# Performance work log

Measured on AMD Instinct MI355X. Metric: run time of the kernel, lower is better.

Reference implementation:

```python
import jax, jax.numpy as jnp
import numpy as np

B, C, H, W = 16, 1536, 32, 32
M = 64      # num_clusters
L = 128     # cluster_dim
G = 256     # token_dim
HID = 512
OT_ITERS = 3
EPS = 1e-6


def setup_inputs() -> dict:
    key = jax.random.key(0)
    ks = jax.random.split(key, 12)
    def w(k, shape, fan_in):
        return jax.random.normal(k, shape, jnp.float32) * (1.0 / np.sqrt(fan_in))
    return {
        'x': jax.random.normal(ks[0], (B, C, H, W), jnp.float32),
        't': jax.random.normal(ks[1], (B, C), jnp.float32),
        # token_features: Linear(C->512), ReLU, Linear(512->G)
        'Wt1': w(ks[2], (HID, C), C), 'bt1': jnp.zeros((HID,), jnp.float32),
        'Wt2': w(ks[3], (G, HID), HID), 'bt2': jnp.zeros((G,), jnp.float32),
        # cluster_features: 1x1 Conv(C->512), ReLU, 1x1 Conv(512->L)
        'Wc1': w(ks[4], (HID, C), C), 'bc1': jnp.zeros((HID,), jnp.float32),
        'Wc2': w(ks[5], (L, HID), HID), 'bc2': jnp.zeros((L,), jnp.float32),
        # score: 1x1 Conv(C->512), ReLU, 1x1 Conv(512->M)
        'Ws1': w(ks[6], (HID, C), C), 'bs1': jnp.zeros((HID,), jnp.float32),
        'Ws2': w(ks[7], (M, HID), HID), 'bs2': jnp.zeros((M,), jnp.float32),
        # temp_predictor: Conv1d(L->1, k=1)
        'Wtp': w(ks[8], (L,), L), 'btp': jnp.zeros((), jnp.float32),
        'dust_bin': jnp.asarray(1.0, jnp.float32),
        'burst_b': jnp.asarray(0.0, jnp.float32),
        'burst_p': jnp.asarray(1.0, jnp.float32),
        'lambda_discount': jnp.asarray(0.5, jnp.float32),
    }


def _log_optimal_transport(scores, alpha, iters):
    # scores: [B, m, n]; alpha: scalar dust-bin logit
    b, m, n = scores.shape
    Z0 = jnp.concatenate([scores, jnp.broadcast_to(alpha, (b, 1, n))], axis=1)  # [B, m+1, n]
    norm = -jnp.log(jnp.asarray(m + n, scores.dtype))
    log_mu = jnp.concatenate([jnp.full((m,), norm, scores.dtype),
                              (jnp.log(jnp.asarray(n, scores.dtype)) + norm)[None]])  # [m+1]
    log_nu = jnp.full((n,), norm, scores.dtype)
    u = jnp.zeros((b, m + 1), scores.dtype)
    v = jnp.zeros((b, n), scores.dtype)
    for _ in range(iters):
        u = log_mu - jax.nn.logsumexp(Z0 + v[:, None, :], axis=2)
        v = log_nu - jax.nn.logsumexp(Z0 + u[:, :, None], axis=1)
    return Z0 + u[:, :, None] + v[:, None, :] - norm


def _l2norm(a, axis):
    return a / jnp.maximum(jnp.linalg.norm(a, axis=axis, keepdims=True), 1e-12)


def _forward(x, t, Wt1, bt1, Wt2, bt2, Wc1, bc1, Wc2, bc2, Ws1, bs1, Ws2, bs2,
             Wtp, btp, dust_bin, burst_b, burst_p, lambda_discount):
    b, c, h, w = x.shape
    n = h * w
    xf = x.reshape(b, c, n)  # [B, C, N] (1x1 convs == per-pixel MLP)
    # cluster features f: [B, L, N]
    h1 = jax.nn.relu(jnp.einsum('bcn,oc->bon', xf, Wc1) + bc1[:, None])
    f = jnp.einsum('bhn,lh->bln', h1, Wc2) + bc2[:, None]
    # assignment scores p: [B, M, N]
    h2 = jax.nn.relu(jnp.einsum('bcn,oc->bon', xf, Ws1) + bs1[:, None])
    p = jnp.einsum('bhn,mh->bmn', h2, Ws2) + bs2[:, None]
    # global token: [B, G]
    tok = jax.nn.relu(t @ Wt1.T + bt1) @ Wt2.T + bt2
    # Sinkhorn OT soft assignment, drop dust bin row
    P = jnp.exp(_log_optimal_transport(p, dust_bin, OT_ITERS))[:, :-1, :]  # [B, M, N]
    # burst-aware weighting
    f_norm = _l2norm(f, axis=1)                                  # [B, L, N]
    T_i = jax.nn.softplus(jnp.einsum('bln,l->bn', f, Wtp) + btp)  # [B, N]
    sim = jnp.einsum('bli,blj->bij', f_norm, f_norm)              # [B, N, N]
    T_avg = (T_i[:, :, None] + T_i[:, None, :]) * 0.5
    burst_w = jax.nn.sigmoid(T_avg * sim + burst_b)
    discount = jnp.clip(jnp.sum(burst_w, axis=-1) ** burst_p, 1e-3, 1e3)  # [B, N]
    lam = jax.nn.sigmoid(lambda_discount)
    P_adj = (1.0 - lam) * P + lam * (P / (discount[:, None, :] + EPS))
    # local aggregation: (f[:, :, None, :] * P[:, None, :, :]).sum(-1) == batched matmul
    agg = jnp.einsum('bln,bmn->blm', f, P_adj)  # [B, L, M]
    agg = _l2norm(agg, axis=1).reshape(b, -1)   # [B, L*M]
    tok_n = _l2norm(tok, axis=-1)
    g = jnp.concatenate([tok_n, agg], axis=-1)  # [B, G + L*M]
    return _l2norm(g, axis=-1)


def reference(x, t, Wt1, bt1, Wt2, bt2, Wc1, bc1, Wc2, bc2, Ws1, bs1, Ws2, bs2,
              Wtp, btp, dust_bin, burst_b, burst_p, lambda_discount):
    return _forward(x, t, Wt1, bt1, Wt2, bt2, Wc1, bc1, Wc2, bc2, Ws1, bs1, Ws2, bs2,
                    Wtp, btp, dust_bin, burst_b, burst_p, lambda_discount)
```

## Files before the change

### kernel.cpp

```cpp
#include <hip/hip_runtime.h>
#include <math.h>

#define B_   16
#define C_   1536
#define N_   1024
#define M_   64
#define L_   128
#define G_   256
#define HID_ 512

typedef __attribute__((ext_vector_type(8))) short short8;
typedef __attribute__((ext_vector_type(4))) float floatx4;

__device__ __forceinline__ unsigned short f2bf_rne(float x) {
    unsigned u = __float_as_uint(x);
    unsigned r = u + 0x7fffu + ((u >> 16) & 1u);
    return (unsigned short)(r >> 16);
}
__device__ __forceinline__ unsigned pack_bf2(float lo, float hi) {
    unsigned a = __float_as_uint(lo) + 0x8000u;
    unsigned b = __float_as_uint(hi) + 0x8000u;
    return (a >> 16) | (b & 0xffff0000u);
}

__device__ __forceinline__ void gl2lds16(const void* g, void* l) {
    __builtin_amdgcn_global_load_lds(
        (const __attribute__((address_space(1))) void*)g,
        (__attribute__((address_space(3))) void*)l, 16, 0, 0);
}

__global__ __launch_bounds__(256) void cast_w_kernel(
    const float* __restrict__ Wc1, const float* __restrict__ Ws1,
    const float* __restrict__ Wc2, const float* __restrict__ Ws2,
    unsigned short* __restrict__ Wbf, unsigned short* __restrict__ W2)
{
    const int T1 = 1024 * 1536;
    int idx = blockIdx.x * 256 + threadIdx.x;
    if (idx < T1) {
        float v = (idx < 512 * 1536) ? Wc1[idx] : Ws1[idx - 512 * 1536];
        Wbf[idx] = f2bf_rne(v);
    } else if (idx < T1 + 192 * 1024) {
        int i2 = idx - T1;
        int row = i2 >> 10, k = i2 & 1023;
        float v = 0.f;
        if (row < 128) { if (k < 512) v = Wc2[row * 512 + k]; }
        else           { if (k >= 512) v = Ws2[(row - 128) * 512 + (k - 512)]; }
        W2[i2] = f2bf_rne(v);
    }
}

__global__ __launch_bounds__(256) void xt_kernel(
    const float* __restrict__ x, unsigned short* __restrict__ xT, int bofs)
{
    __shared__ float Xs[64][65];
    const int t = threadIdx.x;
    const int n0 = blockIdx.x * 64, c0 = blockIdx.y * 64, bl = blockIdx.z;
    const float* xb = x + (long)(bofs + bl) * C_ * N_;
    #pragma unroll
    for (int it = 0; it < 16; ++it) {
        int idx = it * 256 + t, cr = idx >> 6, nc = idx & 63;
        Xs[cr][nc] = xb[(long)(c0 + cr) * N_ + n0 + nc];
    }
    __syncthreads();
    unsigned* xo = (unsigned*)(xT + (long)bl * N_ * C_);
    #pragma unroll
    for (int it = 0; it < 8; ++it) {
        int idx = it * 256 + t, nr = idx >> 5, pc = idx & 31;
        xo[(long)(n0 + nr) * 768 + (c0 >> 1) + pc] =
            pack_bf2(Xs[2 * pc][nr], Xs[2 * pc + 1][nr]);
    }
}

__global__ __launch_bounds__(256, 2) void gemm1_kernel(
    const unsigned short* __restrict__ Wbf, const unsigned short* __restrict__ xT,
    const float* __restrict__ bc1, const float* __restrict__ bs1,
    unsigned short* __restrict__ hT, int bofs)
{
    __shared__ unsigned short As[128 * 32];
    __shared__ unsigned short Bs[128 * 32];
    const int t = threadIdx.x;
    const int lane = t & 63, w = t >> 6;
    const int n0 = blockIdx.x * 128, o0 = blockIdx.y * 128;
    const int bl = blockIdx.z, bg = bofs + bl;
    const unsigned short* xb = xT + (long)bl * N_ * C_;

    const int wo = (w >> 1) * 64, wn = (w & 1) * 64;
    const int lrow = lane & 15, kgrp = lane >> 4;
    const int arow = t >> 2, acol = (t & 3) * 8;

    floatx4 acc[4][4];
    #pragma unroll
    for (int i = 0; i < 4; ++i)
        #pragma unroll
        for (int j = 0; j < 4; ++j) acc[i][j] = (floatx4)0.0f;

    for (int k0 = 0; k0 < C_; k0 += 32) {
        #pragma unroll
        for (int r = 0; r < 2; ++r)
            gl2lds16(Wbf + (long)(o0 + r * 64 + arow) * C_ + k0 + acol,
                     (char*)As + r * 4096 + t * 16);
        #pragma unroll
        for (int r = 0; r < 2; ++r)
            gl2lds16(xb + (long)(n0 + r * 64 + arow) * C_ + k0 + acol,
                     (char*)Bs + r * 4096 + t * 16);
        __syncthreads();
        short8 af[4], bfr[4];
        #pragma unroll
        for (int i = 0; i < 4; ++i)
            af[i] = *(const short8*)((const char*)As +
                        (wo + i * 16 + lrow) * 64 + kgrp * 16);
        #pragma unroll
        for (int j = 0; j < 4; ++j)
            bfr[j] = *(const short8*)((const char*)Bs +
                        (wn + j * 16 + lrow) * 64 + kgrp * 16);
        #pragma unroll
        for (int i = 0; i < 4; ++i)
            #pragma unroll
            for (int j = 0; j < 4; ++j)
                acc[i][j] = __builtin_amdgcn_mfma_f32_16x16x32_bf16(
                    af[i], bfr[j], acc[i][j], 0, 0, 0);
        __syncthreads();
    }

    const float* bias = (o0 < 512) ? bc1 : bs1;
    const int ob = (o0 < 512) ? o0 : o0 - 512;
    #pragma unroll
    for (int i = 0; i < 4; ++i) {
        int orow = wo + i * 16 + kgrp * 4;
        float b0 = bias[ob + orow + 0], b1 = bias[ob + orow + 1];
        float b2 = bias[ob + orow + 2], b3 = bias[ob + orow + 3];
        #pragma unroll
        for (int j = 0; j < 4; ++j) {
            int n = n0 + wn + j * 16 + lrow;
            float v0 = fmaxf(acc[i][j][0] + b0, 0.f);
            float v1 = fmaxf(acc[i][j][1] + b1, 0.f);
            float v2 = fmaxf(acc[i][j][2] + b2, 0.f);
            float v3 = fmaxf(acc[i][j][3] + b3, 0.f);
            uint2 pk;
            pk.x = ((unsigned)f2bf_rne(v0)) | (((unsigned)f2bf_rne(v1)) << 16);
            pk.y = ((unsigned)f2bf_rne(v2)) | (((unsigned)f2bf_rne(v3)) << 16);
            *(uint2*)&hT[((long)bg * N_ + n) * 1024 + o0 + orow] = pk;
        }
    }
}

__global__ __launch_bounds__(256, 2) void gemm23_kernel(
    const unsigned short* __restrict__ W2, const unsigned short* __restrict__ hT,
    const float* __restrict__ bc2, const float* __restrict__ bs2,
    float* __restrict__ f, float* __restrict__ p)
{
    __shared__ unsigned short As[64 * 32];
    __shared__ unsigned short Bs[128 * 32];
    const int t = threadIdx.x;
    const int lane = t & 63, w = t >> 6;
    const int n0 = blockIdx.x * 128, o0 = blockIdx.y * 64, b = blockIdx.z;
    const unsigned short* hTb = hT + (long)b * N_ * 1024;

    const int wo = (w >> 1) * 32, wn = (w & 1) * 64;
    const int lrow = lane & 15, kgrp = lane >> 4;
    const int arow = t >> 2, acol = (t & 3) * 8;

    floatx4 acc[2][4];
    #pragma unroll
    for (int i = 0; i < 2; ++i)
        #pragma unroll
        for (int j = 0; j < 4; ++j) acc[i][j] = (floatx4)0.0f;

    for (int k0 = 0; k0 < 1024; k0 += 32) {
        gl2lds16(W2 + (long)(o0 + arow) * 1024 + k0 + acol, (char*)As + t * 16);
        #pragma unroll
        for (int r = 0; r < 2; ++r)
            gl2lds16(hTb + (long)(n0 + r * 64 + arow) * 1024 + k0 + acol,
                     (char*)Bs + r * 4096 + t * 16);
        __syncthreads();
        short8 af[2], bfr[4];
        #pragma unroll
        for (int i = 0; i < 2; ++i)
            af[i] = *(const short8*)((const char*)As +
                        (wo + i * 16 + lrow) * 64 + kgrp * 16);
        #pragma unroll
        for (int j = 0; j < 4; ++j)
            bfr[j] = *(const short8*)((const char*)Bs +
                        (wn + j * 16 + lrow) * 64 + kgrp * 16);
        #pragma unroll
        for (int i = 0; i < 2; ++i)
            #pragma unroll
            for (int j = 0; j < 4; ++j)
                acc[i][j] = __builtin_amdgcn_mfma_f32_16x16x32_bf16(
                    af[i], bfr[j], acc[i][j], 0, 0, 0);
        __syncthreads();
    }

    #pragma unroll
    for (int i = 0; i < 2; ++i) {
        int o = o0 + wo + i * 16 + kgrp * 4;
        #pragma unroll
        for (int j = 0; j < 4; ++j) {
            int n = n0 + wn + j * 16 + lrow;
            #pragma unroll
            for (int r = 0; r < 4; ++r) {
                int oo = o + r;
                float v = acc[i][j][r];
                if (oo < 128) f[((long)b * L_ + oo) * N_ + n] = v + bc2[oo];
                else p[((long)b * M_ + (oo - 128)) * N_ + n] = v + bs2[oo - 128];
            }
        }
    }
}

__global__ __launch_bounds__(256) void token1_kernel(
    const float* __restrict__ t_in, const float* __restrict__ Wt1,
    const float* __restrict__ bt1, float* __restrict__ hid)
{
    const int lane = threadIdx.x & 63, w = threadIdx.x >> 6;
    const int o = blockIdx.x * 4 + w, b = blockIdx.y;
    const float4* wr = (const float4*)(Wt1 + (long)o * C_);
    const float4* tb = (const float4*)(t_in + (long)b * C_);
    float acc = 0.f;
    #pragma unroll
    for (int i = 0; i < 6; ++i) {
        float4 a = wr[i * 64 + lane], tv = tb[i * 64 + lane];
        acc += a.x * tv.x + a.y * tv.y + a.z * tv.z + a.w * tv.w;
    }
    #pragma unroll
    for (int off = 1; off < 64; off <<= 1) acc += __shfl_xor(acc, off);
    if (lane == 0) hid[b * HID_ + o] = fmaxf(acc + bt1[o], 0.f);
}

__global__ __launch_bounds__(256) void token2_kernel(
    const float* __restrict__ hid, const float* __restrict__ Wt2,
    const float* __restrict__ bt2, float* __restrict__ tok)
{
    const int lane = threadIdx.x & 63, w = threadIdx.x >> 6;
    const int g = blockIdx.x * 4 + w, b = blockIdx.y;
    const float4* wr = (const float4*)(Wt2 + (long)g * HID_);
    const float4* hb = (const float4*)(hid + (long)b * HID_);
    float acc = 0.f;
    #pragma unroll
    for (int i = 0; i < 2; ++i) {
        float4 a = wr[i * 64 + lane], hv = hb[i * 64 + lane];
        acc += a.x * hv.x + a.y * hv.y + a.z * hv.z + a.w * hv.w;
    }
    #pragma unroll
    for (int off = 1; off < 64; off <<= 1) acc += __shfl_xor(acc, off);
    if (lane == 0) tok[b * G_ + g] = acc + bt2[g];
}

__global__ __launch_bounds__(256) void token3_kernel(
    const float* __restrict__ tok, float* __restrict__ tokn)
{
    __shared__ float red[4];
    const int b = blockIdx.x, t = threadIdx.x;
    float v = tok[b * G_ + t];
    float ss = v * v;
    #pragma unroll
    for (int off = 1; off < 64; off <<= 1) ss += __shfl_xor(ss, off);
    if ((t & 63) == 0) red[t >> 6] = ss;
    __syncthreads();
    float inv = 1.f / fmaxf(sqrtf(red[0] + red[1] + red[2] + red[3]), 1e-12f);
    tokn[b * G_ + t] = v * inv;
}

template<bool FIRST>
__global__ __launch_bounds__(256) void ku_kernel(
    const float* __restrict__ p, const float* __restrict__ dust,
    const float* __restrict__ bvec, float* __restrict__ avec)
{
    const int t = threadIdx.x, lane = t & 63, w = t >> 6;
    const int m = blockIdx.x * 4 + w, b = blockIdx.y;
    if (m > M_) return;
    const float* bv = bvec + b * N_;
    float s = 0.f;
    if (m < M_) {
        const float* row = p + ((long)b * M_ + m) * N_;
        #pragma unroll
        for (int i = 0; i < 16; ++i) {
            int n = i * 64 + lane;
            float K = expf(row[n]);
            s += FIRST ? K : K * bv[n];
        }
    } else {
        float ea = expf(dust[0]);
        if (FIRST) s = 16.f * ea;
        else {
            #pragma unroll
            for (int i = 0; i < 16; ++i) s += bv[i * 64 + lane];
            s *= ea;
        }
    }
    #pragma unroll
    for (int off = 1; off < 64; off <<= 1) s += __shfl_xor(s, off);
    if (lane == 0) {
        float mu = (m < M_) ? (1.f / 1088.f) : (1024.f / 1088.f);
        avec[b * (M_ + 1) + m] = mu / s;
    }
}

__global__ __launch_bounds__(256) void kv_kernel(
    const float* __restrict__ p, const float* __restrict__ dust,
    const float* __restrict__ avec, float* __restrict__ bvec)
{
    __shared__ float a_s[M_ + 1];
    const int t = threadIdx.x, b = blockIdx.y;
    const int n = blockIdx.x * 256 + t;
    if (t < M_ + 1) a_s[t] = avec[b * (M_ + 1) + t];
    __syncthreads();
    float s = expf(dust[0]) * a_s[M_];
    const float* col = p + (long)b * M_ * N_ + n;
    #pragma unroll
    for (int m = 0; m < M_; ++m) s = fmaf(expf(col[(long)m * N_]), a_s[m], s);
    bvec[b * N_ + n] = (1.f / 1088.f) / s;
}

__global__ __launch_bounds__(256) void tnorm_kernel(
    const float* __restrict__ f, const float* __restrict__ Wtp,
    const float* __restrict__ btp, unsigned short* __restrict__ fnT,
    float* __restrict__ T, float* __restrict__ draw)
{
    __shared__ float Ft[L_][65];
    __shared__ float invs[64];
    __shared__ float wtp_s[L_];
    const int b = blockIdx.y, n0 = blockIdx.x * 64, t = threadIdx.x;
    const float* fb = f + (long)b * L_ * N_;

    if (t < L_) wtp_s[t] = Wtp[t];
    for (int it = 0; it < 32; ++it) {
        int idx = it * 256 + t;
        int l = idx >> 6, c = idx & 63;
        Ft[l][c] = fb[(long)l * N_ + n0 + c];
    }
    __syncthreads();
    if (t < 64) {
        float ss = 0.f, dot = 0.f;
        #pragma unroll
        for (int l = 0; l < L_; ++l) {
            float v = Ft[l][t];
            ss = fmaf(v, v, ss);
            dot = fmaf(v, wtp_s[l], dot);
        }
        invs[t] = 1.f / fmaxf(sqrtf(ss), 1e-12f);
        float xx = dot + btp[0];
        T[b * N_ + n0 + t] = (xx > 0.f) ? (xx + log1pf(expf(-xx)))
                                        : log1pf(expf(xx));
        draw[b * N_ + n0 + t] = 0.f;
    }
    __syncthreads();
    unsigned* fo = (unsigned*)fnT;
    for (int it = 0; it < 16; ++it) {
        int idx = it * 256 + t;
        int nl = idx >> 6, jp = idx & 63;
        float inv = invs[nl];
        fo[(((long)b * N_ + n0 + nl) << 6) + jp] =
            pack_bf2(Ft[2 * jp][nl] * inv, Ft[2 * jp + 1][nl] * inv);
    }
}

__global__ __launch_bounds__(256) void sim_kernel(
    const unsigned short* __restrict__ fnT, const float* __restrict__ T,
    const float* __restrict__ bb, float* __restrict__ draw)
{
    __shared__ unsigned short As[64 * 136];
    __shared__ unsigned short Bs[64 * 136];
    __shared__ float Ti[64], Tj[64];
    const int b = blockIdx.z, i0 = blockIdx.y * 64, j0 = blockIdx.x * 64;
    const int t = threadIdx.x, lane = t & 63, w = t >> 6;
    const int lrow = lane & 15, kgrp = lane >> 4;
    const unsigned short* fb = fnT + (long)b * N_ * 128;

    if (t < 64) Ti[t] = T[b * N_ + i0 + t];
    else if (t < 128) Tj[t - 64] = T[b * N_ + j0 + (t - 64)];

    const int srow = t >> 4, scol = (t & 15) * 8;
    #pragma unroll
    for (int r = 0; r < 4; ++r) {
        uint4 av = *(const uint4*)(fb + (long)(i0 + r * 16 + srow) * 128 + scol);
        uint4 bv = *(const uint4*)(fb + (long)(j0 + r * 16 + srow) * 128 + scol);
        *(uint4*)((char*)As + (r * 16 + srow) * 272 + scol * 2) = av;
        *(uint4*)((char*)Bs + (r * 16 + srow) * 272 + scol * 2) = bv;
    }
    __syncthreads();

    floatx4 acc[4];
    #pragma unroll
    for (int j = 0; j < 4; ++j) acc[j] = (floatx4)0.0f;
    #pragma unroll
    for (int k0 = 0; k0 < 128; k0 += 32) {
        short8 af = *(const short8*)((const char*)As +
                        (w * 16 + lrow) * 272 + k0 * 2 + kgrp * 16);
        #pragma unroll
        for (int j = 0; j < 4; ++j) {
            short8 bf = *(const short8*)((const char*)Bs +
                            (j * 16 + lrow) * 272 + k0 * 2 + kgrp * 16);
            acc[j] = __builtin_amdgcn_mfma_f32_16x16x32_bf16(af, bf, acc[j], 0, 0, 0);
        }
    }

    const float burstb = bb[0];
    float rs[4] = {0.f, 0.f, 0.f, 0.f};
    #pragma unroll
    for (int j = 0; j < 4; ++j) {
        float Tjv = Tj[j * 16 + lrow];
        #pragma unroll
        for (int r = 0; r < 4; ++r) {
            float Tiv = Ti[w * 16 + kgrp * 4 + r];
            float xarg = 0.5f * (Tiv + Tjv) * acc[j][r] + burstb;
            rs[r] += 1.f / (1.f + expf(-xarg));
        }
    }
    #pragma unroll
    for (int off = 1; off < 16; off <<= 1)
        #pragma unroll
        for (int r = 0; r < 4; ++r) rs[r] += __shfl_xor(rs[r], off);
    if (lrow == 0) {
        #pragma unroll
        for (int r = 0; r < 4; ++r)
            atomicAdd(&draw[b * N_ + i0 + w * 16 + kgrp * 4 + r], rs[r]);
    }
}

__global__ __launch_bounds__(256) void wn_kernel(
    const float* __restrict__ draw, const float* __restrict__ bp,
    const float* __restrict__ lamd, float* __restrict__ wn,
    float* __restrict__ agg)
{
    const int id = blockIdx.x * 256 + threadIdx.x;
    float d = powf(draw[id], bp[0]);
    d = fminf(fmaxf(d, 1e-3f), 1e3f);
    float lam = 1.f / (1.f + expf(-lamd[0]));
    wn[id] = (1.f - lam) + lam / (d + 1e-6f);
    for (int i = id; i < B_ * L_ * M_; i += B_ * N_) agg[i] = 0.f;
}

__global__ __launch_bounds__(256) void agg_kernel(
    const float* __restrict__ f, const float* __restrict__ praw,
    const float* __restrict__ avec, const float* __restrict__ bvec,
    const float* __restrict__ wn, float* __restrict__ agg)
{
    __shared__ float fch[L_][65];
    __shared__ float Pch[M_][65];
    __shared__ float a_s[M_], cf[64];
    const int b = blockIdx.y, n0 = blockIdx.x * 64;
    const int t = threadIdx.x, tx = t & 15, ty = t >> 4;
    const float* fb = f + (long)b * L_ * N_;
    const float* Pb = praw + (long)b * M_ * N_;

    if (t < 64) {
        a_s[t] = avec[b * (M_ + 1) + t] * 1088.f;
        cf[t]  = bvec[b * N_ + n0 + t] * wn[b * N_ + n0 + t];
    }
    __syncthreads();

    for (int idx = t; idx < L_ * 64; idx += 256) {
        int l = idx >> 6, c = idx & 63;
        fch[l][c] = fb[(long)l * N_ + n0 + c];
    }
    for (int idx = t; idx < M_ * 64; idx += 256) {
        int m = idx >> 6, c = idx & 63;
        Pch[m][c] = expf(Pb[(long)m * N_ + n0 + c]) * a_s[m] * cf[c];
    }
    __syncthreads();

    float acc[8][4] = {};
    for (int n = 0; n < 64; ++n) {
        float fv[8], pv[4];
        #pragma unroll
        for (int i = 0; i < 8; ++i) fv[i] = fch[ty + 16 * i][n];
        #pragma unroll
        for (int j = 0; j < 4; ++j) pv[j] = Pch[tx * 4 + j][n];
        #pragma unroll
        for (int i = 0; i < 8; ++i)
            #pragma unroll
            for (int j = 0; j < 4; ++j)
                acc[i][j] = fmaf(fv[i], pv[j], acc[i][j]);
    }
    #pragma unroll
    for (int i = 0; i < 8; ++i)
        #pragma unroll
        for (int j = 0; j < 4; ++j)
            atomicAdd(&agg[((long)b * L_ + (ty + 16 * i)) * M_ + tx * 4 + j],
                      acc[i][j]);
}

__global__ __launch_bounds__(256) void final_kernel(
    const float* __restrict__ tokn, const float* __restrict__ agg,
    float* __restrict__ out)
{
    __shared__ float invm[M_];
    __shared__ float red[4];
    __shared__ float s_invtot;
    const int b = blockIdx.x, t = threadIdx.x;
    const float* ab = agg + (long)b * L_ * M_;

    if (t < 64) {
        float ss = 0.f;
        for (int l = 0; l < L_; ++l) {
            float v = ab[l * M_ + t];
            ss = fmaf(v, v, ss);
        }
        invm[t] = 1.f / fmaxf(sqrtf(ss), 1e-12f);
    }
    __syncthreads();

    float part;
    {
        float tn = tokn[b * G_ + t];
        part = tn * tn;
    }
    for (int idx = t; idx < L_ * M_; idx += 256) {
        float v = ab[idx] * invm[idx & 63];
        part = fmaf(v, v, part);
    }
    for (int off = 32; off; off >>= 1) part += __shfl_down(part, off);
    if ((t & 63) == 0) red[t >> 6] = part;
    __syncthreads();
    if (t == 0)
        s_invtot = 1.f / fmaxf(sqrtf(red[0] + red[1] + red[2] + red[3]), 1e-12f);
    __syncthreads();

    const float invtot = s_invtot;
    float* ob = out + (long)b * (G_ + L_ * M_);
    ob[t] = tokn[b * G_ + t] * invtot;
    for (int idx = t; idx < L_ * M_; idx += 256)
        ob[G_ + idx] = ab[idx] * invm[idx & 63] * invtot;
}

extern "C" void kernel_launch(void* const* d_in, const int* in_sizes, int n_in,
                              void* d_out, int out_size, void* d_ws, size_t ws_size,
                              hipStream_t stream)
{
    const float* x    = (const float*)d_in[0];
    const float* t_in = (const float*)d_in[1];
    const float* Wt1  = (const float*)d_in[2];
    const float* bt1  = (const float*)d_in[3];
    const float* Wt2  = (const float*)d_in[4];
    const float* bt2  = (const float*)d_in[5];
    const float* Wc1  = (const float*)d_in[6];
    const float* bc1  = (const float*)d_in[7];
    const float* Wc2  = (const float*)d_in[8];
    const float* bc2  = (const float*)d_in[9];
    const float* Ws1  = (const float*)d_in[10];
    const float* bs1  = (const float*)d_in[11];
    const float* Ws2  = (const float*)d_in[12];
    const float* bs2  = (const float*)d_in[13];
    const float* Wtp  = (const float*)d_in[14];
    const float* btp  = (const float*)d_in[15];
    const float* dust = (const float*)d_in[16];
    const float* bb   = (const float*)d_in[17];
    const float* bp   = (const float*)d_in[18];
    const float* lamd = (const float*)d_in[19];

    char* wsb = (char*)d_ws;
    unsigned short* xT  = (unsigned short*)wsb;
    float* f    = (float*)(wsb + 0);
    float* p    = (float*)(wsb + 8388608);
    unsigned short* fnT = (unsigned short*)(wsb + 12582912);
    float* hid  = (float*)(wsb + 16777216);
    float* tok  = (float*)(wsb + 16809984);
    float* tokn = (float*)(wsb + 16826368);
    float* T    = (float*)(wsb + 16842752);
    float* draw = (float*)(wsb + 16908288);
    float* wgt  = (float*)(wsb + 16973824);
    float* agg  = (float*)(wsb + 17039360);
    float* avec = (float*)(wsb + 17563648);
    float* bvec = (float*)(wsb + 17567808);
    unsigned short* hT  = (unsigned short*)(wsb + 25165824);
    unsigned short* Wbf = (unsigned short*)(wsb + 58720256);
    unsigned short* W2  = (unsigned short*)(wsb + 61865984);
    float* out  = (float*)d_out;

    cast_w_kernel<<<6912, 256, 0, stream>>>(Wc1, Ws1, Wc2, Ws2, Wbf, W2);

    xt_kernel   <<<dim3(16, 24, 8), 256, 0, stream>>>(x, xT, 0);
    gemm1_kernel<<<dim3(8, 8, 8), 256, 0, stream>>>(Wbf, xT, bc1, bs1, hT, 0);
    xt_kernel   <<<dim3(16, 24, 8), 256, 0, stream>>>(x, xT, 8);
    gemm1_kernel<<<dim3(8, 8, 8), 256, 0, stream>>>(Wbf, xT, bc1, bs1, hT, 8);

    gemm23_kernel<<<dim3(8, 3, 16), 256, 0, stream>>>(W2, hT, bc2, bs2, f, p);

    token1_kernel<<<dim3(128, 16), 256, 0, stream>>>(t_in, Wt1, bt1, hid);
    token2_kernel<<<dim3(64, 16), 256, 0, stream>>>(hid, Wt2, bt2, tok);
    token3_kernel<<<16, 256, 0, stream>>>(tok, tokn);

    ku_kernel<true> <<<dim3(17, 16), 256, 0, stream>>>(p, dust, bvec, avec);
    kv_kernel       <<<dim3(4, 16), 256, 0, stream>>>(p, dust, avec, bvec);
    ku_kernel<false><<<dim3(17, 16), 256, 0, stream>>>(p, dust, bvec, avec);
    kv_kernel       <<<dim3(4, 16), 256, 0, stream>>>(p, dust, avec, bvec);
    ku_kernel<false><<<dim3(17, 16), 256, 0, stream>>>(p, dust, bvec, avec);
    kv_kernel       <<<dim3(4, 16), 256, 0, stream>>>(p, dust, avec, bvec);

    tnorm_kernel<<<dim3(16, 16), 256, 0, stream>>>(f, Wtp, btp, fnT, T, draw);
    sim_kernel  <<<dim3(16, 16, 16), 256, 0, stream>>>(fnT, T, bb, draw);
    wn_kernel   <<<64, 256, 0, stream>>>(draw, bp, lamd, wgt, agg);
    agg_kernel  <<<dim3(16, 16), 256, 0, stream>>>(f, p, avec, bvec, wgt, agg);
    final_kernel<<<16, 256, 0, stream>>>(tokn, agg, out);
}
```

Baseline: 409.7 us.

## Batch gemm1 over all images, cache exp in Sinkhorn, fuse last kv into agg

```diff
diff --git a/kernel.cpp b/kernel.cpp
--- a/kernel.cpp
+++ b/kernel.cpp
@@ -50,19 +50,19 @@
 }
 
 __global__ __launch_bounds__(256) void xt_kernel(
-    const float* __restrict__ x, unsigned short* __restrict__ xT, int bofs)
+    const float* __restrict__ x, unsigned short* __restrict__ xT)
 {
     __shared__ float Xs[64][65];
     const int t = threadIdx.x;
-    const int n0 = blockIdx.x * 64, c0 = blockIdx.y * 64, bl = blockIdx.z;
-    const float* xb = x + (long)(bofs + bl) * C_ * N_;
+    const int n0 = blockIdx.x * 64, c0 = blockIdx.y * 64, b = blockIdx.z;
+    const float* xb = x + (long)b * C_ * N_;
     #pragma unroll
     for (int it = 0; it < 16; ++it) {
         int idx = it * 256 + t, cr = idx >> 6, nc = idx & 63;
         Xs[cr][nc] = xb[(long)(c0 + cr) * N_ + n0 + nc];
     }
     __syncthreads();
-    unsigned* xo = (unsigned*)(xT + (long)bl * N_ * C_);
+    unsigned* xo = (unsigned*)(xT + (long)b * N_ * C_);
     #pragma unroll
     for (int it = 0; it < 8; ++it) {
         int idx = it * 256 + t, nr = idx >> 5, pc = idx & 31;
@@ -74,15 +74,14 @@
 __global__ __launch_bounds__(256, 2) void gemm1_kernel(
     const unsigned short* __restrict__ Wbf, const unsigned short* __restrict__ xT,
     const float* __restrict__ bc1, const float* __restrict__ bs1,
-    unsigned short* __restrict__ hT, int bofs)
+    unsigned short* __restrict__ hT)
 {
     __shared__ unsigned short As[128 * 32];
     __shared__ unsigned short Bs[128 * 32];
     const int t = threadIdx.x;
     const int lane = t & 63, w = t >> 6;
-    const int n0 = blockIdx.x * 128, o0 = blockIdx.y * 128;
-    const int bl = blockIdx.z, bg = bofs + bl;
-    const unsigned short* xb = xT + (long)bl * N_ * C_;
+    const int n0 = blockIdx.x * 128, o0 = blockIdx.y * 128, b = blockIdx.z;
+    const unsigned short* xb = xT + (long)b * N_ * C_;
 
     const int wo = (w >> 1) * 64, wn = (w & 1) * 64;
     const int lrow = lane & 15, kgrp = lane >> 4;
@@ -139,7 +138,7 @@
             uint2 pk;
             pk.x = ((unsigned)f2bf_rne(v0)) | (((unsigned)f2bf_rne(v1)) << 16);
             pk.y = ((unsigned)f2bf_rne(v2)) | (((unsigned)f2bf_rne(v3)) << 16);
-            *(uint2*)&hT[((long)bg * N_ + n) * 1024 + o0 + orow] = pk;
+            *(uint2*)&hT[((long)b * N_ + n) * 1024 + o0 + orow] = pk;
         }
     }
 }
@@ -263,7 +262,7 @@
 
 template<bool FIRST>
 __global__ __launch_bounds__(256) void ku_kernel(
-    const float* __restrict__ p, const float* __restrict__ dust,
+    float* __restrict__ p, const float* __restrict__ dust,
     const float* __restrict__ bvec, float* __restrict__ avec)
 {
     const int t = threadIdx.x, lane = t & 63, w = t >> 6;
@@ -272,12 +271,17 @@
     const float* bv = bvec + b * N_;
     float s = 0.f;
     if (m < M_) {
-        const float* row = p + ((long)b * M_ + m) * N_;
+        float* row = p + ((long)b * M_ + m) * N_;
         #pragma unroll
         for (int i = 0; i < 16; ++i) {
             int n = i * 64 + lane;
-            float K = expf(row[n]);
-            s += FIRST ? K : K * bv[n];
+            if (FIRST) {
+                float K = expf(row[n]);
+                row[n] = K;
+                s += K;
+            } else {
+                s += row[n] * bv[n];
+            }
         }
     } else {
         float ea = expf(dust[0]);
@@ -297,7 +301,7 @@
 }
 
 __global__ __launch_bounds__(256) void kv_kernel(
-    const float* __restrict__ p, const float* __restrict__ dust,
+    const float* __restrict__ K, const float* __restrict__ dust,
     const float* __restrict__ avec, float* __restrict__ bvec)
 {
     __shared__ float a_s[M_ + 1];
@@ -306,9 +310,9 @@
     if (t < M_ + 1) a_s[t] = avec[b * (M_ + 1) + t];
     __syncthreads();
     float s = expf(dust[0]) * a_s[M_];
-    const float* col = p + (long)b * M_ * N_ + n;
-    #pragma unroll
-    for (int m = 0; m < M_; ++m) s = fmaf(expf(col[(long)m * N_]), a_s[m], s);
+    const float* col = K + (long)b * M_ * N_ + n;
+    #pragma unroll
+    for (int m = 0; m < M_; ++m) s = fmaf(col[(long)m * N_], a_s[m], s);
     bvec[b * N_ + n] = (1.f / 1088.f) / s;
 }
 
@@ -362,51 +366,58 @@
     __shared__ unsigned short As[64 * 136];
     __shared__ unsigned short Bs[64 * 136];
     __shared__ float Ti[64], Tj[64];
-    const int b = blockIdx.z, i0 = blockIdx.y * 64, j0 = blockIdx.x * 64;
+    const int b = blockIdx.z, i0 = blockIdx.y * 64, j0base = blockIdx.x * 256;
     const int t = threadIdx.x, lane = t & 63, w = t >> 6;
     const int lrow = lane & 15, kgrp = lane >> 4;
     const unsigned short* fb = fnT + (long)b * N_ * 128;
+    const float burstb = bb[0];
 
     if (t < 64) Ti[t] = T[b * N_ + i0 + t];
-    else if (t < 128) Tj[t - 64] = T[b * N_ + j0 + (t - 64)];
-
     const int srow = t >> 4, scol = (t & 15) * 8;
     #pragma unroll
     for (int r = 0; r < 4; ++r) {
         uint4 av = *(const uint4*)(fb + (long)(i0 + r * 16 + srow) * 128 + scol);
-        uint4 bv = *(const uint4*)(fb + (long)(j0 + r * 16 + srow) * 128 + scol);
         *(uint4*)((char*)As + (r * 16 + srow) * 272 + scol * 2) = av;
-        *(uint4*)((char*)Bs + (r * 16 + srow) * 272 + scol * 2) = bv;
-    }
-    __syncthreads();
-
-    floatx4 acc[4];
-    #pragma unroll
-    for (int j = 0; j < 4; ++j) acc[j] = (floatx4)0.0f;
-    #pragma unroll
-    for (int k0 = 0; k0 < 128; k0 += 32) {
-        short8 af = *(const short8*)((const char*)As +
-                        (w * 16 + lrow) * 272 + k0 * 2 + kgrp * 16);
+    }
+
+    float rs[4] = {0.f, 0.f, 0.f, 0.f};
+    for (int jj = 0; jj < 4; ++jj) {
+        const int j0 = j0base + jj * 64;
+        __syncthreads();
+        #pragma unroll
+        for (int r = 0; r < 4; ++r) {
+            uint4 bv = *(const uint4*)(fb + (long)(j0 + r * 16 + srow) * 128 + scol);
+            *(uint4*)((char*)Bs + (r * 16 + srow) * 272 + scol * 2) = bv;
+        }
+        if (t >= 64 && t < 128) Tj[t - 64] = T[b * N_ + j0 + (t - 64)];
+        __syncthreads();
+
+        floatx4 acc[4];
+        #pragma unroll
+        for (int j = 0; j < 4; ++j) acc[j] = (floatx4)0.0f;
+        #pragma unroll
+        for (int k0 = 0; k0 < 128; k0 += 32) {
+            short8 af = *(const short8*)((const char*)As +
+                            (w * 16 + lrow) * 272 + k0 * 2 + kgrp * 16);
+            #pragma unroll
+            for (int j = 0; j < 4; ++j) {
+                short8 bf = *(const short8*)((const char*)Bs +
+                                (j * 16 + lrow) * 272 + k0 * 2 + kgrp * 16);
+                acc[j] = __builtin_amdgcn_mfma_f32_16x16x32_bf16(af, bf, acc[j], 0, 0, 0);
+            }
+        }
         #pragma unroll
         for (int j = 0; j < 4; ++j) {
-            short8 bf = *(const short8*)((const char*)Bs +
-                            (j * 16 + lrow) * 272 + k0 * 2 + kgrp * 16);
-            acc[j] = __builtin_amdgcn_mfma_f32_16x16x32_bf16(af, bf, acc[j], 0, 0, 0);
-        }
-    }
-
-    const float burstb = bb[0];
-    float rs[4] = {0.f, 0.f, 0.f, 0.f};
-    #pragma unroll
-    for (int j = 0; j < 4; ++j) {
-        float Tjv = Tj[j * 16 + lrow];
-        #pragma unroll
-        for (int r = 0; r < 4; ++r) {
-            float Tiv = Ti[w * 16 + kgrp * 4 + r];
-            float xarg = 0.5f * (Tiv + Tjv) * acc[j][r] + burstb;
-            rs[r] += 1.f / (1.f + expf(-xarg));
-        }
-    }
+            float Tjv = Tj[j * 16 + lrow];
+            #pragma unroll
+            for (int r = 0; r < 4; ++r) {
+                float Tiv = Ti[w * 16 + kgrp * 4 + r];
+                float xarg = 0.5f * (Tiv + Tjv) * acc[j][r] + burstb;
+                rs[r] += 1.f / (1.f + expf(-xarg));
+            }
+        }
+    }
+
     #pragma unroll
     for (int off = 1; off < 16; off <<= 1)
         #pragma unroll
@@ -432,22 +443,19 @@
 }
 
 __global__ __launch_bounds__(256) void agg_kernel(
-    const float* __restrict__ f, const float* __restrict__ praw,
-    const float* __restrict__ avec, const float* __restrict__ bvec,
+    const float* __restrict__ f, const float* __restrict__ Kmat,
+    const float* __restrict__ avec, const float* __restrict__ dust,
     const float* __restrict__ wn, float* __restrict__ agg)
 {
     __shared__ float fch[L_][65];
     __shared__ float Pch[M_][65];
-    __shared__ float a_s[M_], cf[64];
+    __shared__ float a_s[M_ + 1], cf[64];
     const int b = blockIdx.y, n0 = blockIdx.x * 64;
     const int t = threadIdx.x, tx = t & 15, ty = t >> 4;
     const float* fb = f + (long)b * L_ * N_;
-    const float* Pb = praw + (long)b * M_ * N_;
-
-    if (t < 64) {
-        a_s[t] = avec[b * (M_ + 1) + t] * 1088.f;
-        cf[t]  = bvec[b * N_ + n0 + t] * wn[b * N_ + n0 + t];
-    }
+    const float* Kb = Kmat + (long)b * M_ * N_;
+
+    if (t < M_ + 1) a_s[t] = avec[b * (M_ + 1) + t];
     __syncthreads();
 
     for (int idx = t; idx < L_ * 64; idx += 256) {
@@ -456,17 +464,26 @@
     }
     for (int idx = t; idx < M_ * 64; idx += 256) {
         int m = idx >> 6, c = idx & 63;
-        Pch[m][c] = expf(Pb[(long)m * N_ + n0 + c]) * a_s[m] * cf[c];
+        Pch[m][c] = Kb[(long)m * N_ + n0 + c] * a_s[m];
+    }
+    __syncthreads();
+
+    if (t < 64) {
+        float s = expf(dust[0]) * a_s[M_];
+        #pragma unroll
+        for (int m = 0; m < M_; ++m) s += Pch[m][t];
+        cf[t] = wn[b * N_ + n0 + t] / s;
     }
     __syncthreads();
 
     float acc[8][4] = {};
     for (int n = 0; n < 64; ++n) {
+        float cfn = cf[n];
         float fv[8], pv[4];
         #pragma unroll
         for (int i = 0; i < 8; ++i) fv[i] = fch[ty + 16 * i][n];
         #pragma unroll
-        for (int j = 0; j < 4; ++j) pv[j] = Pch[tx * 4 + j][n];
+        for (int j = 0; j < 4; ++j) pv[j] = Pch[tx * 4 + j][n] * cfn;
         #pragma unroll
         for (int i = 0; i < 8; ++i)
             #pragma unroll
@@ -563,18 +580,15 @@
     float* agg  = (float*)(wsb + 17039360);
     float* avec = (float*)(wsb + 17563648);
     float* bvec = (float*)(wsb + 17567808);
-    unsigned short* hT  = (unsigned short*)(wsb + 25165824);
-    unsigned short* Wbf = (unsigned short*)(wsb + 58720256);
-    unsigned short* W2  = (unsigned short*)(wsb + 61865984);
+    unsigned short* hT  = (unsigned short*)(wsb + 50331648);
+    unsigned short* Wbf = (unsigned short*)(wsb + 83886080);
+    unsigned short* W2  = (unsigned short*)(wsb + 87031808);
     float* out  = (float*)d_out;
 
     cast_w_kernel<<<6912, 256, 0, stream>>>(Wc1, Ws1, Wc2, Ws2, Wbf, W2);
 
-    xt_kernel   <<<dim3(16, 24, 8), 256, 0, stream>>>(x, xT, 0);
-    gemm1_kernel<<<dim3(8, 8, 8), 256, 0, stream>>>(Wbf, xT, bc1, bs1, hT, 0);
-    xt_kernel   <<<dim3(16, 24, 8), 256, 0, stream>>>(x, xT, 8);
-    gemm1_kernel<<<dim3(8, 8, 8), 256, 0, stream>>>(Wbf, xT, bc1, bs1, hT, 8);
-
+    xt_kernel   <<<dim3(16, 24, 16), 256, 0, stream>>>(x, xT);
+    gemm1_kernel<<<dim3(8, 8, 16), 256, 0, stream>>>(Wbf, xT, bc1, bs1, hT);
     gemm23_kernel<<<dim3(8, 3, 16), 256, 0, stream>>>(W2, hT, bc2, bs2, f, p);
 
     token1_kernel<<<dim3(128, 16), 256, 0, stream>>>(t_in, Wt1, bt1, hid);
@@ -586,11 +600,10 @@
     ku_kernel<false><<<dim3(17, 16), 256, 0, stream>>>(p, dust, bvec, avec);
     kv_kernel       <<<dim3(4, 16), 256, 0, stream>>>(p, dust, avec, bvec);
     ku_kernel<false><<<dim3(17, 16), 256, 0, stream>>>(p, dust, bvec, avec);
-    kv_kernel       <<<dim3(4, 16), 256, 0, stream>>>(p, dust, avec, bvec);
 
     tnorm_kernel<<<dim3(16, 16), 256, 0, stream>>>(f, Wtp, btp, fnT, T, draw);
-    sim_kernel  <<<dim3(16, 16, 16), 256, 0, stream>>>(fnT, T, bb, draw);
+    sim_kernel  <<<dim3(4, 16, 16), 256, 0, stream>>>(fnT, T, bb, draw);
     wn_kernel   <<<64, 256, 0, stream>>>(draw, bp, lamd, wgt, agg);
-    agg_kernel  <<<dim3(16, 16), 256, 0, stream>>>(f, p, avec, bvec, wgt, agg);
+    agg_kernel  <<<dim3(16, 16), 256, 0, stream>>>(f, p, avec, dust, wgt, agg);
     final_kernel<<<16, 256, 0, stream>>>(tokn, agg, out);
 }
```

Measured after the change: 391.0 us. -4.6%, faster.
